# Kernel tuning notes

Measured on AMD Instinct MI355X. Metric: run time of the kernel, lower is better.

The kernel has to match this reference:

```python
import jax, jax.numpy as jnp
import numpy as np

B, T, D = 2, 2048, 1024
E, H, K = 8, 2048, 2  # n_experts, expert_dim, n_active_experts


def setup_inputs() -> dict:
    key = jax.random.key(0)
    ks = jax.random.split(key, 5)
    s = 0.02
    return {
        "x": jax.random.normal(ks[0], (B, T, D), dtype=jnp.float32),
        "gate_w": jax.random.normal(ks[1], (E, D), dtype=jnp.float32) * s,
        "w1": jax.random.normal(ks[2], (E, H, D), dtype=jnp.float32) * s,
        "w2": jax.random.normal(ks[3], (E, D, H), dtype=jnp.float32) * s,
        "w3": jax.random.normal(ks[4], (E, H, D), dtype=jnp.float32) * s,
    }


def reference(x, gate_w, w1, w2, w3):
    Bb, Tt, Dd = x.shape
    xf = x.reshape(-1, Dd)                       # [N, D]
    logits = xf @ gate_w.T                       # [N, E]
    probs = jax.nn.softmax(logits, axis=-1)
    vals, idx = jax.lax.top_k(probs, K)          # [N, K]
    w = vals / (vals.sum(-1, keepdims=True) + 1e-8)
    onehot = jax.nn.one_hot(idx, E, dtype=xf.dtype)  # [N, K, E]
    comb = jnp.einsum('nk,nke->ne', w, onehot)   # per-token per-expert combine weight
    # Dense expert eval (same math as masked loop): SwiGLU per expert
    h = jnp.einsum('nd,ehd->neh', xf, w1)        # [N, E, H]
    g = jnp.einsum('nd,ehd->neh', xf, w3)
    eo = jnp.einsum('neh,edh->ned', jax.nn.silu(h) * g, w2)  # [N, E, D]
    out = jnp.einsum('ned,ne->nd', eo, comb)
    return out.reshape(Bb, Tt, Dd)
```

## Files before the change

kernel.cpp:

```cpp
#include <hip/hip_runtime.h>
#include <stdint.h>

#define N_TOK 4096
#define DIM   1024
#define NEXP  8
#define HDIM  2048
#define NSLOT 8192

typedef __attribute__((ext_vector_type(8))) short  short8;
typedef __attribute__((ext_vector_type(4))) float  f32x4;

__device__ inline unsigned short f2bf(float f) {
  union { float f; uint32_t u; } v; v.f = f;
  uint32_t u = v.u;
  u += 0x7fffu + ((u >> 16) & 1u);
  return (unsigned short)(u >> 16);
}

__device__ inline void gload_lds16(const void* g, void* l) {
  __builtin_amdgcn_global_load_lds(
      (const __attribute__((address_space(1))) uint32_t*)g,
      (__attribute__((address_space(3))) uint32_t*)l, 16, 0, 0);
}

__global__ __launch_bounds__(256) void cvt_kernel(const float* __restrict__ s,
                                                  unsigned short* __restrict__ d,
                                                  int n4) {
  int i = blockIdx.x * blockDim.x + threadIdx.x;
  int stride = gridDim.x * blockDim.x;
  for (; i < n4; i += stride) {
    float4 f = reinterpret_cast<const float4*>(s)[i];
    ushort4 o;
    o.x = f2bf(f.x); o.y = f2bf(f.y); o.z = f2bf(f.z); o.w = f2bf(f.w);
    reinterpret_cast<ushort4*>(d)[i] = o;
  }
}

__global__ __launch_bounds__(256) void gate_kernel(const float* __restrict__ x,
                                                   const float* __restrict__ gw,
                                                   int* __restrict__ tok_e,
                                                   float* __restrict__ tok_w) {
  __shared__ float gws[NEXP * DIM];
  int tid = threadIdx.x;
  for (int i = tid; i < NEXP * DIM; i += 256) gws[i] = gw[i];
  __syncthreads();
  int lane = tid & 63;
  int token = blockIdx.x * 4 + (tid >> 6);
  const float* xr = x + (size_t)token * DIM;
  float acc[NEXP];
#pragma unroll
  for (int e = 0; e < NEXP; ++e) acc[e] = 0.f;
  for (int i = 0; i < DIM / 64; ++i) {
    float xv = xr[i * 64 + lane];
#pragma unroll
    for (int e = 0; e < NEXP; ++e) acc[e] += xv * gws[e * DIM + i * 64 + lane];
  }
#pragma unroll
  for (int off = 32; off > 0; off >>= 1) {
#pragma unroll
    for (int e = 0; e < NEXP; ++e) acc[e] += __shfl_xor(acc[e], off);
  }
  if (lane == 0) {
    float m = acc[0];
#pragma unroll
    for (int e = 1; e < NEXP; ++e) m = fmaxf(m, acc[e]);
    float ex[NEXP], Z = 0.f;
#pragma unroll
    for (int e = 0; e < NEXP; ++e) { ex[e] = expf(acc[e] - m); Z += ex[e]; }
    int b0 = 0; float v0 = ex[0];
#pragma unroll
    for (int e = 1; e < NEXP; ++e) if (ex[e] > v0) { v0 = ex[e]; b0 = e; }
    int b1 = -1; float v1 = -1.f;
#pragma unroll
    for (int e = 0; e < NEXP; ++e) if (e != b0 && ex[e] > v1) { v1 = ex[e]; b1 = e; }
    float p0 = v0 / Z, p1 = v1 / Z;
    float s = p0 + p1 + 1e-8f;
    tok_e[token * 2 + 0] = b0; tok_e[token * 2 + 1] = b1;
    tok_w[token * 2 + 0] = p0 / s; tok_w[token * 2 + 1] = p1 / s;
  }
}

__global__ __launch_bounds__(1024) void route_kernel(const int* __restrict__ tok_e,
                                                     const float* __restrict__ tok_w,
                                                     int* __restrict__ slot_tok,
                                                     float* __restrict__ slot_w,
                                                     int* __restrict__ cnt_g,
                                                     int* __restrict__ offs_g) {
  __shared__ int cnt[NEXP], offs[NEXP], cur[NEXP];
  int tid = threadIdx.x;
  if (tid < NEXP) cnt[tid] = 0;
  __syncthreads();
  for (int n = tid; n < N_TOK; n += 1024) {
    atomicAdd(&cnt[tok_e[2 * n]], 1);
    atomicAdd(&cnt[tok_e[2 * n + 1]], 1);
  }
  __syncthreads();
  if (tid == 0) {
    int o = 0;
    for (int e = 0; e < NEXP; ++e) { offs[e] = o; cur[e] = o; o += cnt[e]; }
    for (int e = 0; e < NEXP; ++e) { cnt_g[e] = cnt[e]; offs_g[e] = offs[e]; }
  }
  __syncthreads();
  for (int n = tid; n < N_TOK; n += 1024) {
#pragma unroll
    for (int k = 0; k < 2; ++k) {
      int e = tok_e[2 * n + k];
      int p = atomicAdd(&cur[e], 1);
      slot_tok[p] = n;
      slot_w[p] = tok_w[2 * n + k];
    }
  }
}

__global__ __launch_bounds__(256) void gemm1_kernel(const unsigned short* __restrict__ xb,
                                                    const unsigned short* __restrict__ w1b,
                                                    const unsigned short* __restrict__ w3b,
                                                    const int* __restrict__ slot_tok,
                                                    const int* __restrict__ cnt_g,
                                                    const int* __restrict__ offs_g,
                                                    unsigned short* __restrict__ hidden) {
  const int ROWT = N_TOK / 128;
  const int COLT = HDIM / 128;
  int bid = blockIdx.x;
  int e  = bid / (ROWT * COLT);
  int rt = (bid / COLT) % ROWT;
  int ct = bid % COLT;
  int cnt = cnt_g[e];
  if (rt * 128 >= cnt) return;
  int rowBase = offs_g[e] + rt * 128;

  __shared__ alignas(16) unsigned short As[128 * 64];
  __shared__ alignas(16) unsigned short B1s[128 * 64];
  __shared__ alignas(16) unsigned short B3s[128 * 64];
  __shared__ int toks[128];

  int tid = threadIdx.x;
  if (tid < 128) {
    int slot = rowBase + tid; if (slot > NSLOT - 1) slot = NSLOT - 1;
    toks[tid] = slot_tok[slot];
  }
  __syncthreads();

  int wave = tid >> 6, lane = tid & 63;
  int wr = (wave >> 1) * 64, wc = (wave & 1) * 64;
  int lrow = lane >> 3, lcol = (lane & 7) * 8;

  f32x4 hacc[4][4], gacc[4][4];
#pragma unroll
  for (int m = 0; m < 4; ++m)
#pragma unroll
    for (int n = 0; n < 4; ++n) {
      hacc[m][n] = (f32x4){0.f, 0.f, 0.f, 0.f};
      gacc[m][n] = (f32x4){0.f, 0.f, 0.f, 0.f};
    }

  const size_t wbase = (size_t)e * HDIM * DIM;
  for (int kt = 0; kt < DIM / 64; ++kt) {
    int k0 = kt * 64;
#pragma unroll
    for (int i = 0; i < 4; ++i) {
      int row = i * 32 + wave * 8 + lrow;
      gload_lds16(xb + (size_t)toks[row] * DIM + k0 + lcol, &As[(i * 32 + wave * 8) * 64]);
      gload_lds16(w1b + wbase + (size_t)(ct * 128 + row) * DIM + k0 + lcol, &B1s[(i * 32 + wave * 8) * 64]);
      gload_lds16(w3b + wbase + (size_t)(ct * 128 + row) * DIM + k0 + lcol, &B3s[(i * 32 + wave * 8) * 64]);
    }
    asm volatile("s_waitcnt vmcnt(0)" ::: "memory");
    __syncthreads();
#pragma unroll
    for (int ks = 0; ks < 2; ++ks) {
      int ko = ks * 32 + (lane >> 4) * 8;
      short8 a[4], b1[4], b3[4];
#pragma unroll
      for (int m = 0; m < 4; ++m)
        a[m] = *(const short8*)&As[(wr + m * 16 + (lane & 15)) * 64 + ko];
#pragma unroll
      for (int n = 0; n < 4; ++n) {
        b1[n] = *(const short8*)&B1s[(wc + n * 16 + (lane & 15)) * 64 + ko];
        b3[n] = *(const short8*)&B3s[(wc + n * 16 + (lane & 15)) * 64 + ko];
      }
#pragma unroll
      for (int m = 0; m < 4; ++m)
#pragma unroll
        for (int n = 0; n < 4; ++n) {
          hacc[m][n] = __builtin_amdgcn_mfma_f32_16x16x32_bf16(a[m], b1[n], hacc[m][n], 0, 0, 0);
          gacc[m][n] = __builtin_amdgcn_mfma_f32_16x16x32_bf16(a[m], b3[n], gacc[m][n], 0, 0, 0);
        }
    }
    __syncthreads();
  }

  int cbase = ct * 128 + wc;
#pragma unroll
  for (int m = 0; m < 4; ++m) {
#pragma unroll
    for (int q = 0; q < 4; ++q) {
      int r = wr + m * 16 + ((lane >> 4) * 4 + q);
      if (rt * 128 + r < cnt) {
        size_t rowoff = (size_t)(rowBase + r) * HDIM + cbase;
#pragma unroll
        for (int n = 0; n < 4; ++n) {
          float h = hacc[m][n][q], g = gacc[m][n][q];
          float val = (h / (1.f + expf(-h))) * g;
          hidden[rowoff + n * 16 + (lane & 15)] = f2bf(val);
        }
      }
    }
  }
}

__global__ __launch_bounds__(256) void gemm2_kernel(const unsigned short* __restrict__ hidden,
                                                    const unsigned short* __restrict__ w2b,
                                                    const int* __restrict__ slot_tok,
                                                    const float* __restrict__ slot_w,
                                                    const int* __restrict__ cnt_g,
                                                    const int* __restrict__ offs_g,
                                                    float* __restrict__ out) {
  const int ROWT = N_TOK / 128;
  const int COLT = DIM / 128;
  int bid = blockIdx.x;
  int e  = bid / (ROWT * COLT);
  int rt = (bid / COLT) % ROWT;
  int ct = bid % COLT;
  int cnt = cnt_g[e];
  if (rt * 128 >= cnt) return;
  int rowBase = offs_g[e] + rt * 128;

  __shared__ alignas(16) unsigned short As[128 * 64];
  __shared__ alignas(16) unsigned short Bs[128 * 64];
  __shared__ int   toks[128];
  __shared__ float wgt[128];

  int tid = threadIdx.x;
  if (tid < 128) {
    int slot = rowBase + tid; if (slot > NSLOT - 1) slot = NSLOT - 1;
    toks[tid] = slot_tok[slot];
    wgt[tid]  = slot_w[slot];
  }
  __syncthreads();

  int wave = tid >> 6, lane = tid & 63;
  int wr = (wave >> 1) * 64, wc = (wave & 1) * 64;
  int lrow = lane >> 3, lcol = (lane & 7) * 8;

  f32x4 acc[4][4];
#pragma unroll
  for (int m = 0; m < 4; ++m)
#pragma unroll
    for (int n = 0; n < 4; ++n) acc[m][n] = (f32x4){0.f, 0.f, 0.f, 0.f};

  const size_t w2base = (size_t)e * DIM * HDIM;
  for (int kt = 0; kt < HDIM / 64; ++kt) {
    int k0 = kt * 64;
#pragma unroll
    for (int i = 0; i < 4; ++i) {
      int row = i * 32 + wave * 8 + lrow;
      int rg = rowBase + row; if (rg > NSLOT - 1) rg = NSLOT - 1;
      gload_lds16(hidden + (size_t)rg * HDIM + k0 + lcol, &As[(i * 32 + wave * 8) * 64]);
      gload_lds16(w2b + w2base + (size_t)(ct * 128 + row) * HDIM + k0 + lcol, &Bs[(i * 32 + wave * 8) * 64]);
    }
    asm volatile("s_waitcnt vmcnt(0)" ::: "memory");
    __syncthreads();
#pragma unroll
    for (int ks = 0; ks < 2; ++ks) {
      int ko = ks * 32 + (lane >> 4) * 8;
      short8 a[4], b[4];
#pragma unroll
      for (int m = 0; m < 4; ++m)
        a[m] = *(const short8*)&As[(wr + m * 16 + (lane & 15)) * 64 + ko];
#pragma unroll
      for (int n = 0; n < 4; ++n)
        b[n] = *(const short8*)&Bs[(wc + n * 16 + (lane & 15)) * 64 + ko];
#pragma unroll
      for (int m = 0; m < 4; ++m)
#pragma unroll
        for (int n = 0; n < 4; ++n)
          acc[m][n] = __builtin_amdgcn_mfma_f32_16x16x32_bf16(a[m], b[n], acc[m][n], 0, 0, 0);
    }
    __syncthreads();
  }

  int cbase = ct * 128 + wc;
#pragma unroll
  for (int m = 0; m < 4; ++m) {
#pragma unroll
    for (int q = 0; q < 4; ++q) {
      int r = wr + m * 16 + ((lane >> 4) * 4 + q);
      if (rt * 128 + r < cnt) {
        float w = wgt[r];
        float* orow = out + (size_t)toks[r] * DIM + cbase;
#pragma unroll
        for (int n = 0; n < 4; ++n)
          unsafeAtomicAdd(&orow[n * 16 + (lane & 15)], acc[m][n][q] * w);
      }
    }
  }
}

extern "C" void kernel_launch(void* const* d_in, const int* in_sizes, int n_in,
                              void* d_out, int out_size, void* d_ws, size_t ws_size,
                              hipStream_t stream) {
  const float* x  = (const float*)d_in[0];
  const float* gw = (const float*)d_in[1];
  const float* w1 = (const float*)d_in[2];
  const float* w2 = (const float*)d_in[3];
  const float* w3 = (const float*)d_in[4];
  float* out = (float*)d_out;

  uint8_t* ws = (uint8_t*)d_ws;
  size_t off = 0;
  auto alloc = [&](size_t bytes) -> void* {
    void* p = ws + off; off += (bytes + 255) & ~255ull; return p;
  };
  unsigned short* xb     = (unsigned short*)alloc((size_t)N_TOK * DIM * 2);
  unsigned short* w1b    = (unsigned short*)alloc((size_t)NEXP * HDIM * DIM * 2);
  unsigned short* w3b    = (unsigned short*)alloc((size_t)NEXP * HDIM * DIM * 2);
  unsigned short* w2b    = (unsigned short*)alloc((size_t)NEXP * DIM * HDIM * 2);
  unsigned short* hidden = (unsigned short*)alloc((size_t)NSLOT * HDIM * 2);
  int*   tok_e    = (int*)alloc(N_TOK * 2 * 4);
  float* tok_w    = (float*)alloc(N_TOK * 2 * 4);
  int*   slot_tok = (int*)alloc(NSLOT * 4);
  float* slot_w   = (float*)alloc(NSLOT * 4);
  int*   cnt_g    = (int*)alloc(NEXP * 4);
  int*   offs_g   = (int*)alloc(NEXP * 4);

  hipMemsetAsync(d_out, 0, (size_t)out_size * sizeof(float), stream);

  cvt_kernel<<<2048, 256, 0, stream>>>(x,  xb,  N_TOK * DIM / 4);
  cvt_kernel<<<2048, 256, 0, stream>>>(w1, w1b, NEXP * HDIM * DIM / 4);
  cvt_kernel<<<2048, 256, 0, stream>>>(w3, w3b, NEXP * HDIM * DIM / 4);
  cvt_kernel<<<2048, 256, 0, stream>>>(w2, w2b, NEXP * DIM * HDIM / 4);

  gate_kernel<<<N_TOK / 4, 256, 0, stream>>>(x, gw, tok_e, tok_w);
  route_kernel<<<1, 1024, 0, stream>>>(tok_e, tok_w, slot_tok, slot_w, cnt_g, offs_g);
  gemm1_kernel<<<NEXP * (N_TOK / 128) * (HDIM / 128), 256, 0, stream>>>(
      xb, w1b, w3b, slot_tok, cnt_g, offs_g, hidden);
  gemm2_kernel<<<NEXP * (N_TOK / 128) * (DIM / 128), 256, 0, stream>>>(
      hidden, w2b, slot_tok, slot_w, cnt_g, offs_g, out);
}
```

Measured before the change: 559.9 us.

## Double-buffer LDS with XOR swizzle and 256-row tiles in expert GEMMs

Both expert GEMM kernels now prefetch the next K tile into a second LDS buffer while the current one is computed, and apply an XOR swizzle to the LDS column layout to avoid bank conflicts on the fragment reads. gemm1 uses 512-thread blocks covering 256 token rows, so each weight tile is reused across twice as many tokens, and launch bounds are raised to allow two blocks per CU. The trade-off is higher LDS use per block and more register pressure, which can limit occupancy. Row-tile coverage drops from 32 to 16 tiles per expert, which holds only while per-expert token counts stay at or below 4096.

```diff
diff --git a/kernel.cpp b/kernel.cpp
--- a/kernel.cpp
+++ b/kernel.cpp
@@ -112,38 +112,56 @@
   }
 }
 
-__global__ __launch_bounds__(256) void gemm1_kernel(const unsigned short* __restrict__ xb,
-                                                    const unsigned short* __restrict__ w1b,
-                                                    const unsigned short* __restrict__ w3b,
-                                                    const int* __restrict__ slot_tok,
-                                                    const int* __restrict__ cnt_g,
-                                                    const int* __restrict__ offs_g,
-                                                    unsigned short* __restrict__ hidden) {
-  const int ROWT = N_TOK / 128;
+__global__ __launch_bounds__(512, 2) void gemm1_kernel(const unsigned short* __restrict__ xb,
+                                                       const unsigned short* __restrict__ w1b,
+                                                       const unsigned short* __restrict__ w3b,
+                                                       const int* __restrict__ slot_tok,
+                                                       const int* __restrict__ cnt_g,
+                                                       const int* __restrict__ offs_g,
+                                                       unsigned short* __restrict__ hidden) {
+  const int ROWT = 16;
   const int COLT = HDIM / 128;
   int bid = blockIdx.x;
   int e  = bid / (ROWT * COLT);
   int rt = (bid / COLT) % ROWT;
   int ct = bid % COLT;
   int cnt = cnt_g[e];
-  if (rt * 128 >= cnt) return;
-  int rowBase = offs_g[e] + rt * 128;
-
-  __shared__ alignas(16) unsigned short As[128 * 64];
-  __shared__ alignas(16) unsigned short B1s[128 * 64];
-  __shared__ alignas(16) unsigned short B3s[128 * 64];
-  __shared__ int toks[128];
+  if (rt * 256 >= cnt) return;
+  int rowBase = offs_g[e] + rt * 256;
+
+  __shared__ alignas(16) unsigned short As[2][256 * 64];
+  __shared__ alignas(16) unsigned short B1s[2][128 * 64];
+  __shared__ alignas(16) unsigned short B3s[2][128 * 64];
+  __shared__ int toks[256];
 
   int tid = threadIdx.x;
-  if (tid < 128) {
+  if (tid < 256) {
     int slot = rowBase + tid; if (slot > NSLOT - 1) slot = NSLOT - 1;
     toks[tid] = slot_tok[slot];
   }
   __syncthreads();
 
   int wave = tid >> 6, lane = tid & 63;
-  int wr = (wave >> 1) * 64, wc = (wave & 1) * 64;
-  int lrow = lane >> 3, lcol = (lane & 7) * 8;
+  int wr = (wave >> 1) * 64;
+  int wc = (wave & 1) * 64;
+  int sub = lane >> 3;
+  int swcol = (((lane & 7) ^ sub) << 3);
+
+  const size_t wbase = (size_t)e * HDIM * DIM;
+  const unsigned short* aptr[4];
+  const unsigned short* b1ptr[2];
+  const unsigned short* b3ptr[2];
+#pragma unroll
+  for (int i = 0; i < 4; ++i) {
+    int r = (wave + i * 8) * 8 + sub;
+    aptr[i] = xb + (size_t)toks[r] * DIM + swcol;
+  }
+#pragma unroll
+  for (int i = 0; i < 2; ++i) {
+    int r = (wave + i * 8) * 8 + sub;
+    b1ptr[i] = w1b + wbase + (size_t)(ct * 128 + r) * DIM + swcol;
+    b3ptr[i] = w3b + wbase + (size_t)(ct * 128 + r) * DIM + swcol;
+  }
 
   f32x4 hacc[4][4], gacc[4][4];
 #pragma unroll
@@ -154,39 +172,50 @@
       gacc[m][n] = (f32x4){0.f, 0.f, 0.f, 0.f};
     }
 
-  const size_t wbase = (size_t)e * HDIM * DIM;
-  for (int kt = 0; kt < DIM / 64; ++kt) {
+  auto stage = [&](int b, int kt) {
     int k0 = kt * 64;
 #pragma unroll
-    for (int i = 0; i < 4; ++i) {
-      int row = i * 32 + wave * 8 + lrow;
-      gload_lds16(xb + (size_t)toks[row] * DIM + k0 + lcol, &As[(i * 32 + wave * 8) * 64]);
-      gload_lds16(w1b + wbase + (size_t)(ct * 128 + row) * DIM + k0 + lcol, &B1s[(i * 32 + wave * 8) * 64]);
-      gload_lds16(w3b + wbase + (size_t)(ct * 128 + row) * DIM + k0 + lcol, &B3s[(i * 32 + wave * 8) * 64]);
+    for (int i = 0; i < 4; ++i)
+      gload_lds16(aptr[i] + k0, &As[b][(wave + i * 8) * 512]);
+#pragma unroll
+    for (int i = 0; i < 2; ++i) {
+      gload_lds16(b1ptr[i] + k0, &B1s[b][(wave + i * 8) * 512]);
+      gload_lds16(b3ptr[i] + k0, &B3s[b][(wave + i * 8) * 512]);
+    }
+  };
+
+  const int NKT = DIM / 64;
+  stage(0, 0);
+  asm volatile("s_waitcnt vmcnt(0)" ::: "memory");
+  __syncthreads();
+
+  int key = (lane & 7) << 3;
+  for (int kt = 0; kt < NKT; ++kt) {
+    int cur = kt & 1;
+    if (kt + 1 < NKT) stage(cur ^ 1, kt + 1);
+#pragma unroll
+    for (int ks = 0; ks < 2; ++ks) {
+      int kg = ks * 32 + (lane >> 4) * 8;
+      int pc = kg ^ key;
+      short8 a[4], b1v[4], b3v[4];
+#pragma unroll
+      for (int m = 0; m < 4; ++m)
+        a[m] = *(const short8*)&As[cur][(wr + m * 16 + (lane & 15)) * 64 + pc];
+#pragma unroll
+      for (int n = 0; n < 4; ++n) {
+        b1v[n] = *(const short8*)&B1s[cur][(wc + n * 16 + (lane & 15)) * 64 + pc];
+        b3v[n] = *(const short8*)&B3s[cur][(wc + n * 16 + (lane & 15)) * 64 + pc];
+      }
+#pragma unroll
+      for (int m = 0; m < 4; ++m)
+#pragma unroll
+        for (int n = 0; n < 4; ++n) {
+          hacc[m][n] = __builtin_amdgcn_mfma_f32_16x16x32_bf16(a[m], b1v[n], hacc[m][n], 0, 0, 0);
+          gacc[m][n] = __builtin_amdgcn_mfma_f32_16x16x32_bf16(a[m], b3v[n], gacc[m][n], 0, 0, 0);
+        }
     }
     asm volatile("s_waitcnt vmcnt(0)" ::: "memory");
     __syncthreads();
-#pragma unroll
-    for (int ks = 0; ks < 2; ++ks) {
-      int ko = ks * 32 + (lane >> 4) * 8;
-      short8 a[4], b1[4], b3[4];
-#pragma unroll
-      for (int m = 0; m < 4; ++m)
-        a[m] = *(const short8*)&As[(wr + m * 16 + (lane & 15)) * 64 + ko];
-#pragma unroll
-      for (int n = 0; n < 4; ++n) {
-        b1[n] = *(const short8*)&B1s[(wc + n * 16 + (lane & 15)) * 64 + ko];
-        b3[n] = *(const short8*)&B3s[(wc + n * 16 + (lane & 15)) * 64 + ko];
-      }
-#pragma unroll
-      for (int m = 0; m < 4; ++m)
-#pragma unroll
-        for (int n = 0; n < 4; ++n) {
-          hacc[m][n] = __builtin_amdgcn_mfma_f32_16x16x32_bf16(a[m], b1[n], hacc[m][n], 0, 0, 0);
-          gacc[m][n] = __builtin_amdgcn_mfma_f32_16x16x32_bf16(a[m], b3[n], gacc[m][n], 0, 0, 0);
-        }
-    }
-    __syncthreads();
   }
 
   int cbase = ct * 128 + wc;
@@ -195,7 +224,7 @@
 #pragma unroll
     for (int q = 0; q < 4; ++q) {
       int r = wr + m * 16 + ((lane >> 4) * 4 + q);
-      if (rt * 128 + r < cnt) {
+      if (rt * 256 + r < cnt) {
         size_t rowoff = (size_t)(rowBase + r) * HDIM + cbase;
 #pragma unroll
         for (int n = 0; n < 4; ++n) {
@@ -208,14 +237,14 @@
   }
 }
 
-__global__ __launch_bounds__(256) void gemm2_kernel(const unsigned short* __restrict__ hidden,
-                                                    const unsigned short* __restrict__ w2b,
-                                                    const int* __restrict__ slot_tok,
-                                                    const float* __restrict__ slot_w,
-                                                    const int* __restrict__ cnt_g,
-                                                    const int* __restrict__ offs_g,
-                                                    float* __restrict__ out) {
-  const int ROWT = N_TOK / 128;
+__global__ __launch_bounds__(256, 2) void gemm2_kernel(const unsigned short* __restrict__ hidden,
+                                                       const unsigned short* __restrict__ w2b,
+                                                       const int* __restrict__ slot_tok,
+                                                       const float* __restrict__ slot_w,
+                                                       const int* __restrict__ cnt_g,
+                                                       const int* __restrict__ offs_g,
+                                                       float* __restrict__ out) {
+  const int ROWT = 32;
   const int COLT = DIM / 128;
   int bid = blockIdx.x;
   int e  = bid / (ROWT * COLT);
@@ -225,8 +254,8 @@
   if (rt * 128 >= cnt) return;
   int rowBase = offs_g[e] + rt * 128;
 
-  __shared__ alignas(16) unsigned short As[128 * 64];
-  __shared__ alignas(16) unsigned short Bs[128 * 64];
+  __shared__ alignas(16) unsigned short As[2][128 * 64];
+  __shared__ alignas(16) unsigned short Bs[2][128 * 64];
   __shared__ int   toks[128];
   __shared__ float wgt[128];
 
@@ -240,7 +269,19 @@
 
   int wave = tid >> 6, lane = tid & 63;
   int wr = (wave >> 1) * 64, wc = (wave & 1) * 64;
-  int lrow = lane >> 3, lcol = (lane & 7) * 8;
+  int sub = lane >> 3;
+  int swcol = (((lane & 7) ^ sub) << 3);
+
+  const size_t w2base = (size_t)e * DIM * HDIM;
+  const unsigned short* aptr[4];
+  const unsigned short* bptr[4];
+#pragma unroll
+  for (int i = 0; i < 4; ++i) {
+    int r = (wave + i * 4) * 8 + sub;
+    int rg = rowBase + r; if (rg > NSLOT - 1) rg = NSLOT - 1;
+    aptr[i] = hidden + (size_t)rg * HDIM + swcol;
+    bptr[i] = w2b + w2base + (size_t)(ct * 128 + r) * HDIM + swcol;
+  }
 
   f32x4 acc[4][4];
 #pragma unroll
@@ -248,34 +289,42 @@
 #pragma unroll
     for (int n = 0; n < 4; ++n) acc[m][n] = (f32x4){0.f, 0.f, 0.f, 0.f};
 
-  const size_t w2base = (size_t)e * DIM * HDIM;
-  for (int kt = 0; kt < HDIM / 64; ++kt) {
+  auto stage = [&](int b, int kt) {
     int k0 = kt * 64;
 #pragma unroll
     for (int i = 0; i < 4; ++i) {
-      int row = i * 32 + wave * 8 + lrow;
-      int rg = rowBase + row; if (rg > NSLOT - 1) rg = NSLOT - 1;
-      gload_lds16(hidden + (size_t)rg * HDIM + k0 + lcol, &As[(i * 32 + wave * 8) * 64]);
-      gload_lds16(w2b + w2base + (size_t)(ct * 128 + row) * HDIM + k0 + lcol, &Bs[(i * 32 + wave * 8) * 64]);
-    }
-    asm volatile("s_waitcnt vmcnt(0)" ::: "memory");
-    __syncthreads();
+      gload_lds16(aptr[i] + k0, &As[b][(wave + i * 4) * 512]);
+      gload_lds16(bptr[i] + k0, &Bs[b][(wave + i * 4) * 512]);
+    }
+  };
+
+  const int NKT = HDIM / 64;
+  stage(0, 0);
+  asm volatile("s_waitcnt vmcnt(0)" ::: "memory");
+  __syncthreads();
+
+  int key = (lane & 7) << 3;
+  for (int kt = 0; kt < NKT; ++kt) {
+    int cur = kt & 1;
+    if (kt + 1 < NKT) stage(cur ^ 1, kt + 1);
 #pragma unroll
     for (int ks = 0; ks < 2; ++ks) {
-      int ko = ks * 32 + (lane >> 4) * 8;
+      int kg = ks * 32 + (lane >> 4) * 8;
+      int pc = kg ^ key;
       short8 a[4], b[4];
 #pragma unroll
       for (int m = 0; m < 4; ++m)
-        a[m] = *(const short8*)&As[(wr + m * 16 + (lane & 15)) * 64 + ko];
+        a[m] = *(const short8*)&As[cur][(wr + m * 16 + (lane & 15)) * 64 + pc];
 #pragma unroll
       for (int n = 0; n < 4; ++n)
-        b[n] = *(const short8*)&Bs[(wc + n * 16 + (lane & 15)) * 64 + ko];
+        b[n] = *(const short8*)&Bs[cur][(wc + n * 16 + (lane & 15)) * 64 + pc];
 #pragma unroll
       for (int m = 0; m < 4; ++m)
 #pragma unroll
         for (int n = 0; n < 4; ++n)
           acc[m][n] = __builtin_amdgcn_mfma_f32_16x16x32_bf16(a[m], b[n], acc[m][n], 0, 0, 0);
     }
+    asm volatile("s_waitcnt vmcnt(0)" ::: "memory");
     __syncthreads();
   }
 
@@ -332,8 +381,8 @@
 
   gate_kernel<<<N_TOK / 4, 256, 0, stream>>>(x, gw, tok_e, tok_w);
   route_kernel<<<1, 1024, 0, stream>>>(tok_e, tok_w, slot_tok, slot_w, cnt_g, offs_g);
-  gemm1_kernel<<<NEXP * (N_TOK / 128) * (HDIM / 128), 256, 0, stream>>>(
+  gemm1_kernel<<<NEXP * 16 * (HDIM / 128), 512, 0, stream>>>(
       xb, w1b, w3b, slot_tok, cnt_g, offs_g, hidden);
-  gemm2_kernel<<<NEXP * (N_TOK / 128) * (DIM / 128), 256, 0, stream>>>(
+  gemm2_kernel<<<NEXP * 32 * (DIM / 128), 256, 0, stream>>>(
       hidden, w2b, slot_tok, slot_w, cnt_g, offs_g, out);
 }
```

Result: faster. 464.0 us (-17.1%).
